# Performance work log

Hardware: AMD Instinct MI355X
Metric: run time of the kernel (lower is better)

The kernel has to match this reference:

```python
import math
import jax, jax.numpy as jnp
import numpy as np

LOW_FREQ = 1
FACTOR = 1


def setup_inputs() -> dict:
    key = jax.random.key(0)
    x = jax.random.normal(key, (8, 4096, 512), dtype=jnp.float32)
    return {"x": x}


def reference(x):
    b, t, d = x.shape
    x_freq = jnp.fft.rfft(x, axis=1)  # (b, t//2+1, d) complex
    if t % 2 == 0:
        x_freq = x_freq[:, LOW_FREQ:-1]
        f = jnp.fft.rfftfreq(t)[LOW_FREQ:-1]
    else:
        x_freq = x_freq[:, LOW_FREQ:]
        f = jnp.fft.rfftfreq(t)[LOW_FREQ:]
    length = x_freq.shape[1]
    top_k = int(FACTOR * math.log(length))

    # top-k |X(f)| independently per (batch, channel)
    amp_all = jnp.abs(x_freq)                      # (b, F, d)
    _, idx = jax.lax.top_k(jnp.transpose(amp_all, (0, 2, 1)), top_k)  # (b, d, k)
    idx = jnp.transpose(idx, (0, 2, 1))            # (b, k, d)
    x_sel = jnp.take_along_axis(x_freq, idx, axis=1)  # (b, k, d) complex
    f_sel = f[idx].astype(jnp.float32)             # (b, k, d)

    # extrapolate: append conjugate components with negated frequency
    x2 = jnp.concatenate([x_sel, jnp.conj(x_sel)], axis=1)  # (b, 2k, d)
    f2 = jnp.concatenate([f_sel, -f_sel], axis=1)           # (b, 2k, d)
    amp = jnp.abs(x2)[:, :, None, :]               # (b, 2k, 1, d)
    phase = jnp.angle(x2)[:, :, None, :]           # (b, 2k, 1, d)
    tt = jnp.arange(t, dtype=jnp.float32)[None, None, :, None]  # (1,1,t,1)
    x_time = amp * jnp.cos(2.0 * math.pi * f2[:, :, None, :] * tt + phase)  # (b,2k,t,d)
    return jnp.sum(x_time, axis=1)                 # (b, t, d)
```

## Files before the change

### kernel.cpp

```cpp
#include <hip/hip_runtime.h>
#include <math.h>

#define B 8
#define T 4096
#define D 512
#define NPAIR ((B * D) / 2)
#define TOPK 7
#define LOG2T 12
#define PAD(e) ((e) + ((e) >> 4))
#define ZSZ (T + (T >> 4))

__device__ __forceinline__ int brev12(int x) {
  return (int)(__brev((unsigned)x) >> (32 - LOG2T));
}

__global__ __launch_bounds__(256) void k_transpose_pack(const float* __restrict__ x,
                                                        float2* __restrict__ xp) {
  __shared__ float tile[64][65];
  const int b  = blockIdx.z;
  const int t0 = blockIdx.x * 64;
  const int d0 = blockIdx.y * 64;
  const int tx = threadIdx.x;
  const int ty = threadIdx.y;

  for (int r = ty; r < 64; r += 4)
    tile[r][tx] = x[((size_t)b * T + (t0 + r)) * D + (d0 + tx)];
  __syncthreads();
  for (int rp = ty; rp < 32; rp += 4) {
    float2 v = make_float2(tile[tx][2 * rp], tile[tx][2 * rp + 1]);
    xp[((size_t)b * (D / 2) + (d0 / 2 + rp)) * T + (t0 + tx)] = v;
  }
}

__global__ __launch_bounds__(256) void k_fft_topk(float2* __restrict__ xp) {
  __shared__ float2 Z[ZSZ];
  __shared__ float  s_rv[4];
  __shared__ int    s_rk[4];
  __shared__ float4 s_cf[2 * TOPK];

  const int tid = threadIdx.x;
  float2* g = xp + (size_t)blockIdx.x * T;

  for (int t = tid; t < T; t += 256) Z[PAD(t)] = g[t];
  __syncthreads();

  for (int s = 0; s < 6; ++s) {
    const int shift = 10 - 2 * s;
    const int q = 1 << shift;
    const float ang_scale = -6.283185307179586f / (float)(q << 2);
    for (int i = tid; i < T / 4; i += 256) {
      const int p    = i & (q - 1);
      const int base = ((i >> shift) << (shift + 2)) | p;
      float2 a0 = Z[PAD(base)];
      float2 a1 = Z[PAD(base + q)];
      float2 a2 = Z[PAD(base + 2 * q)];
      float2 a3 = Z[PAD(base + 3 * q)];
      float sw, cw;
      __sincosf(ang_scale * (float)p, &sw, &cw);
      const float c2 = cw * cw - sw * sw, s2 = 2.0f * cw * sw;
      const float c3 = c2 * cw - s2 * sw, s3 = c2 * sw + s2 * cw;
      const float t0r = a0.x + a2.x, t0i = a0.y + a2.y;
      const float t1r = a0.x - a2.x, t1i = a0.y - a2.y;
      const float t2r = a1.x + a3.x, t2i = a1.y + a3.y;
      const float t3r = a1.x - a3.x, t3i = a1.y - a3.y;
      Z[PAD(base)] = make_float2(t0r + t2r, t0i + t2i);
      const float u1r = t0r - t2r, u1i = t0i - t2i;
      Z[PAD(base + q)] = make_float2(u1r * c2 - u1i * s2, u1r * s2 + u1i * c2);
      const float u2r = t1r + t3i, u2i = t1i - t3r;
      Z[PAD(base + 2 * q)] = make_float2(u2r * cw - u2i * sw, u2r * sw + u2i * cw);
      const float u3r = t1r - t3i, u3i = t1i + t3r;
      Z[PAD(base + 3 * q)] = make_float2(u3r * c3 - u3i * s3, u3r * s3 + u3i * c3);
    }
    __syncthreads();
  }

  float a1v[8], a2v[8];
  #pragma unroll
  for (int j = 0; j < 8; ++j) {
    const int k = 1 + tid + (j << 8);
    if (k >= T / 2) { a1v[j] = -1e30f; a2v[j] = -1e30f; continue; }
    const float2 zk = Z[PAD(brev12(k))];
    const float2 zn = Z[PAD(brev12(T - k))];
    const float x1r = 0.5f * (zk.x + zn.x), x1i = 0.5f * (zk.y - zn.y);
    const float x2r = 0.5f * (zk.y + zn.y), x2i = 0.5f * (zn.x - zk.x);
    a1v[j] = x1r * x1r + x1i * x1i;
    a2v[j] = x2r * x2r + x2i * x2i;
  }

  for (int sh = 0; sh < 2; ++sh) {
    for (int it = 0; it < TOPK; ++it) {
      float bv = -1e30f;
      int bj = 0;
      #pragma unroll
      for (int j = 0; j < 8; ++j) {
        const float v = (sh == 0) ? a1v[j] : a2v[j];
        if (v > bv) { bv = v; bj = j; }
      }
      int bk = 1 + tid + (bj << 8);
      #pragma unroll
      for (int off = 1; off < 64; off <<= 1) {
        const float ov = __shfl_xor(bv, off);
        const int   ok = __shfl_xor(bk, off);
        if (ov > bv) { bv = ov; bk = ok; }
      }
      if ((tid & 63) == 0) { s_rv[tid >> 6] = bv; s_rk[tid >> 6] = bk; }
      __syncthreads();
      float wv = s_rv[0];
      int   wk = s_rk[0];
      #pragma unroll
      for (int w = 1; w < 4; ++w)
        if (s_rv[w] > wv) { wv = s_rv[w]; wk = s_rk[w]; }
      if (((wk - 1) & 255) == tid) {
        const int j = (wk - 1) >> 8;
        #pragma unroll
        for (int jj = 0; jj < 8; ++jj)
          if (jj == j) { if (sh == 0) a1v[jj] = -1e30f; else a2v[jj] = -1e30f; }
      }
      if (tid == 0) {
        const float2 zk = Z[PAD(brev12(wk))];
        const float2 zn = Z[PAD(brev12(T - wk))];
        float re, im;
        if (sh == 0) { re = 0.5f * (zk.x + zn.x); im = 0.5f * (zk.y - zn.y); }
        else         { re = 0.5f * (zk.y + zn.y); im = 0.5f * (zn.x - zk.x); }
        s_cf[sh * TOPK + it] = make_float4((float)wk, re, im, 0.0f);
      }
      __syncthreads();
    }
  }

  float4* cf = (float4*)g;
  if (tid < 2 * TOPK) cf[tid] = s_cf[tid];
}

__global__ __launch_bounds__(256) void k_eval(const float* __restrict__ ws,
                                              float* __restrict__ out) {
  const int tx = threadIdx.x;
  const int ty = threadIdx.y;
  const int b  = blockIdx.z;
  const int d0 = blockIdx.y * 64;
  const int t0 = blockIdx.x * 256;
  const int d  = d0 + tx;
  const int P  = (b * D + d) >> 1;
  const int sh = d & 1;
  const float4* cf = (const float4*)(ws + (size_t)P * (2 * T)) + sh * TOPK;

  float re[TOPK], im[TOPK], cc[TOPK], ss[TOPK], cd[TOPK], sd[TOPK];
  const int ts = t0 + ty * 64;
  const float w0 = 6.283185307179586f / 4096.0f;
  #pragma unroll
  for (int j = 0; j < TOPK; ++j) {
    const float4 v = cf[j];
    const int k = (int)v.x;
    re[j] = 2.0f * v.y;
    im[j] = 2.0f * v.z;
    const int m0 = (k * ts) & (T - 1);
    __sincosf(w0 * (float)m0, &ss[j], &cc[j]);
    __sincosf(w0 * (float)k,  &sd[j], &cd[j]);
  }
  #pragma unroll 4
  for (int i = 0; i < 64; ++i) {
    float acc = 0.0f;
    #pragma unroll
    for (int j = 0; j < TOPK; ++j) {
      acc += re[j] * cc[j] - im[j] * ss[j];
      const float nc = cc[j] * cd[j] - ss[j] * sd[j];
      const float ns = ss[j] * cd[j] + cc[j] * sd[j];
      cc[j] = nc; ss[j] = ns;
    }
    out[((size_t)b * T + (ts + i)) * D + d] = acc;
  }
}

extern "C" void kernel_launch(void* const* d_in, const int* in_sizes, int n_in,
                              void* d_out, int out_size, void* d_ws, size_t ws_size,
                              hipStream_t stream) {
  const float* x = (const float*)d_in[0];
  float* out = (float*)d_out;
  float2* xp = (float2*)d_ws;

  dim3 tgrid(T / 64, D / 64, B);
  dim3 tblock(64, 4, 1);
  hipLaunchKernelGGL(k_transpose_pack, tgrid, tblock, 0, stream, x, xp);
  hipLaunchKernelGGL(k_fft_topk, dim3(NPAIR), dim3(256), 0, stream, xp);
  dim3 egrid(T / 256, D / 64, B);
  hipLaunchKernelGGL(k_eval, egrid, tblock, 0, stream, (const float*)d_ws, out);
}
```

Baseline: 202.5 us.

## Vectorize transpose and stage eval output through shared memory tile

The transpose-pack kernel now reads float4 rows and writes float4 pairs to the packed layout. The eval kernel now loads coefficients for 64 channels into shared memory and computes a 64x64 time-by-channel tile with interleaved time steps (stride 4 recurrence). It then writes the tile out with coalesced float4 stores. The aim is to widen global memory transactions in both bandwidth-bound kernels, at the cost of extra shared memory traffic, a barrier, and a smaller per-block time range that recomputes sincos more often.

```diff
diff --git a/kernel.cpp b/kernel.cpp
--- a/kernel.cpp
+++ b/kernel.cpp
@@ -16,19 +16,30 @@
 
 __global__ __launch_bounds__(256) void k_transpose_pack(const float* __restrict__ x,
                                                         float2* __restrict__ xp) {
-  __shared__ float tile[64][65];
+  __shared__ float tT[64][65];
   const int b  = blockIdx.z;
   const int t0 = blockIdx.x * 64;
   const int d0 = blockIdx.y * 64;
-  const int tx = threadIdx.x;
-  const int ty = threadIdx.y;
-
-  for (int r = ty; r < 64; r += 4)
-    tile[r][tx] = x[((size_t)b * T + (t0 + r)) * D + (d0 + tx)];
-  __syncthreads();
-  for (int rp = ty; rp < 32; rp += 4) {
-    float2 v = make_float2(tile[tx][2 * rp], tile[tx][2 * rp + 1]);
-    xp[((size_t)b * (D / 2) + (d0 / 2 + rp)) * T + (t0 + tx)] = v;
+  const int tid = threadIdx.x;
+
+  const int c4 = tid & 15;
+  const int r0 = tid >> 4;
+  for (int r = r0; r < 64; r += 16) {
+    const float4 v = *(const float4*)&x[((size_t)b * T + (t0 + r)) * D + d0 + 4 * c4];
+    tT[4 * c4 + 0][r] = v.x;
+    tT[4 * c4 + 1][r] = v.y;
+    tT[4 * c4 + 2][r] = v.z;
+    tT[4 * c4 + 3][r] = v.w;
+  }
+  __syncthreads();
+
+  const int tt  = tid & 31;
+  const int rp0 = tid >> 5;
+  for (int rp = rp0; rp < 32; rp += 8) {
+    const float2 a  = *(const float2*)&tT[2 * rp][2 * tt];
+    const float2 bb = *(const float2*)&tT[2 * rp + 1][2 * tt];
+    const float4 o = make_float4(a.x, bb.x, a.y, bb.y);
+    *(float4*)&xp[((size_t)b * (D / 2) + (d0 / 2 + rp)) * T + t0 + 2 * tt] = o;
   }
 }
 
@@ -134,31 +145,42 @@
 
 __global__ __launch_bounds__(256) void k_eval(const float* __restrict__ ws,
                                               float* __restrict__ out) {
-  const int tx = threadIdx.x;
-  const int ty = threadIdx.y;
-  const int b  = blockIdx.z;
-  const int d0 = blockIdx.y * 64;
-  const int t0 = blockIdx.x * 256;
-  const int d  = d0 + tx;
-  const int P  = (b * D + d) >> 1;
-  const int sh = d & 1;
-  const float4* cf = (const float4*)(ws + (size_t)P * (2 * T)) + sh * TOPK;
+  __shared__ float  tile[64][64];
+  __shared__ float4 s_coef[64 * TOPK];
+
+  const int tid = threadIdx.x;
+  const int b   = blockIdx.z;
+  const int d0  = blockIdx.y * 64;
+  const int t0  = blockIdx.x * 64;
+
+  for (int idx = tid; idx < 64 * TOPK; idx += 256) {
+    const int s = idx / TOPK, j = idx - s * TOPK;
+    const int P = (b * D + d0) / 2 + (s >> 1);
+    const int sh = s & 1;
+    s_coef[idx] = ((const float4*)(ws + (size_t)P * (2 * T)))[sh * TOPK + j];
+  }
+  __syncthreads();
+
+  const int dl = tid & 63;
+  const int tg = tid >> 6;
+  const float w0 = 6.283185307179586f / 4096.0f;
 
   float re[TOPK], im[TOPK], cc[TOPK], ss[TOPK], cd[TOPK], sd[TOPK];
-  const int ts = t0 + ty * 64;
-  const float w0 = 6.283185307179586f / 4096.0f;
+  const int ts = t0 + tg;
   #pragma unroll
   for (int j = 0; j < TOPK; ++j) {
-    const float4 v = cf[j];
+    const float4 v = s_coef[dl * TOPK + j];
     const int k = (int)v.x;
     re[j] = 2.0f * v.y;
     im[j] = 2.0f * v.z;
-    const int m0 = (k * ts) & (T - 1);
-    __sincosf(w0 * (float)m0, &ss[j], &cc[j]);
-    __sincosf(w0 * (float)k,  &sd[j], &cd[j]);
-  }
-  #pragma unroll 4
-  for (int i = 0; i < 64; ++i) {
+    const float a0 = w0 * (float)((k * ts) & (T - 1));
+    const float ad = w0 * (float)((4 * k) & (T - 1));
+    ss[j] = __sinf(a0); cc[j] = __cosf(a0);
+    sd[j] = __sinf(ad); cd[j] = __cosf(ad);
+  }
+
+  #pragma unroll
+  for (int i = 0; i < 16; ++i) {
     float acc = 0.0f;
     #pragma unroll
     for (int j = 0; j < TOPK; ++j) {
@@ -167,7 +189,15 @@
       const float ns = ss[j] * cd[j] + cc[j] * sd[j];
       cc[j] = nc; ss[j] = ns;
     }
-    out[((size_t)b * T + (ts + i)) * D + d] = acc;
+    tile[tg + 4 * i][dl] = acc;
+  }
+  __syncthreads();
+
+  const int c4 = tid & 15;
+  const int rw = tid >> 4;
+  for (int rr = rw; rr < 64; rr += 16) {
+    const float4 v = *(const float4*)&tile[rr][4 * c4];
+    *(float4*)&out[((size_t)b * T + (t0 + rr)) * D + d0 + 4 * c4] = v;
   }
 }
 
@@ -179,9 +209,7 @@
   float2* xp = (float2*)d_ws;
 
   dim3 tgrid(T / 64, D / 64, B);
-  dim3 tblock(64, 4, 1);
-  hipLaunchKernelGGL(k_transpose_pack, tgrid, tblock, 0, stream, x, xp);
+  hipLaunchKernelGGL(k_transpose_pack, tgrid, dim3(256), 0, stream, x, xp);
   hipLaunchKernelGGL(k_fft_topk, dim3(NPAIR), dim3(256), 0, stream, xp);
-  dim3 egrid(T / 256, D / 64, B);
-  hipLaunchKernelGGL(k_eval, egrid, tblock, 0, stream, (const float*)d_ws, out);
-}
+  hipLaunchKernelGGL(k_eval, tgrid, dim3(256), 0, stream, (const float*)d_ws, out);
+}
```

Measured after the change: 201.1 us. About the same (-0.7%).
